# Kernel optimization log

Hardware: AMD Instinct MI355X
Metric: run time of the kernel (lower is better)

## Reference

```python
import jax, jax.numpy as jnp
import numpy as np

B, C, W, H, X, Y = 2, 32, 256, 256, 512, 512


def _rbf(x1, x2, ls):
    # x1: [B, N], x2: [B, M] -> [B, N, M]; identical math to norms+matmul pw_dists2 on 1-d coords
    d2 = (x1[:, :, None] - x2[:, None, :]) ** 2
    return jnp.exp(-0.5 * d2 / ls ** 2)


def setup_inputs() -> dict:
    key = jax.random.key(0)
    k0, k1, k2, k3, k4 = jax.random.split(key, 5)
    return {
        "x_in_lon": jax.random.uniform(k0, (B, W), jnp.float32),
        "x_in_lat": jax.random.uniform(k1, (B, H), jnp.float32),
        "wt": jax.random.normal(k2, (B, C, W, H), jnp.float32),
        "x_out_lon": jax.random.uniform(k3, (B, X), jnp.float32),
        "x_out_lat": jax.random.uniform(k4, (B, Y), jnp.float32),
        "init_ls": jnp.full((1,), 0.1, jnp.float32),
    }


def reference(x_in_lon, x_in_lat, wt, x_out_lon, x_out_lat, init_ls):
    # density channel: 1 where data present, 0 where NaN; zero-fill NaNs in data
    dens = jnp.where(jnp.isnan(wt[:, 0:1]), 0.0, 1.0)
    wt_full = jnp.concatenate([dens, jnp.nan_to_num(wt)], axis=1)  # [B, C+1, W, H]
    ls = init_ls[0]
    w_lon = _rbf(x_in_lon, x_out_lon, ls)  # [B, W, X]
    w_lat = _rbf(x_in_lat, x_out_lat, ls)  # [B, H, Y]
    # separable 'OnToOn' contraction: [B,C+1,W,H] x [B,W,X] x [B,H,Y] -> [B,C+1,X,Y]
    ee = jnp.einsum('bcwh,bwx,bhy->bcxy', wt_full, w_lon, w_lat)
    d = jnp.clip(ee[:, 0:1], 1e-6, 1e5)
    return jnp.concatenate([ee[:, 0:1], ee[:, 1:] / d], axis=1)
```

## Files before the change

### kernel.cpp

```cpp
#include <hip/hip_runtime.h>
#include <cstddef>

#define B_ 2
#define C_ 32
#define CP 33
#define W_ 256
#define H_ 256
#define X_ 512
#define Y_ 512

typedef __bf16 bf16x8 __attribute__((ext_vector_type(8)));
typedef __bf16 bf16x4 __attribute__((ext_vector_type(4)));
typedef float  f32x4  __attribute__((ext_vector_type(4)));

#define AS1 __attribute__((address_space(1)))
#define AS3 __attribute__((address_space(3)))

__device__ __forceinline__ void gload16_lds(const void* g, void* l) {
    __builtin_amdgcn_global_load_lds((const AS1 void*)g, (AS3 void*)l, 16, 0, 0);
}


__global__ __launch_bounds__(256) void prep_kernel(
    const float* __restrict__ xin_lon, const float* __restrict__ xin_lat,
    const float* __restrict__ xout_lon, const float* __restrict__ xout_lat,
    const float* __restrict__ init_ls, const float* __restrict__ wt,
    __bf16* __restrict__ wlonF, __bf16* __restrict__ wlatT,
    __bf16* __restrict__ wt33)
{
    const int NLONC = 32768;
    const int NLAT  = B_ * Y_ * H_;
    int t = blockIdx.x * 256 + threadIdx.x;
    float ls = init_ls[0];
    float cc = -0.5f / (ls * ls);
    if (t < NLONC) {
        int lane = t & 63, nf = (t >> 6) & 3, kt = (t >> 8) & 7;
        int xt = (t >> 11) & 7, b = t >> 14;
        int x  = xt * 64 + nf * 16 + (lane & 15);
        int k0 = kt * 32 + (lane >> 4) * 8;
        float xo = xout_lon[b * X_ + x];
        bf16x8 v;
#pragma unroll
        for (int e = 0; e < 8; ++e) {
            float d = xin_lon[b * W_ + k0 + e] - xo;
            v[e] = (__bf16)__expf(cc * d * d);
        }
        *(bf16x8*)&wlonF[(size_t)t * 8] = v;
    } else if (t < NLONC + NLAT) {
        int j = t - NLONC;
        int b = j / (Y_ * H_);
        int r = j - b * (Y_ * H_);
        int y = r >> 8;
        int h = r & (H_ - 1);
        float d = xin_lat[b * H_ + h] - xout_lat[b * Y_ + y];
        wlatT[j] = (__bf16)__expf(cc * d * d);
    } else {
        int j = t - (NLONC + NLAT);
        if (j >= (B_ * CP * W_ * H_) / 4) return;
        int o = j * 4;
        int b = o / (CP * W_ * H_);
        int r = o - b * (CP * W_ * H_);
        int co = r / (W_ * H_);
        int p = r & (W_ * H_ - 1);
        float4 v;
        bf16x4 ov;
        if (co == 0) {
            v = *(const float4*)&wt[((size_t)b * C_) * (W_ * H_) + p];
            ov[0] = (__bf16)((v.x != v.x) ? 0.f : 1.f);
            ov[1] = (__bf16)((v.y != v.y) ? 0.f : 1.f);
            ov[2] = (__bf16)((v.z != v.z) ? 0.f : 1.f);
            ov[3] = (__bf16)((v.w != v.w) ? 0.f : 1.f);
        } else {
            v = *(const float4*)&wt[((size_t)b * C_ + (co - 1)) * (W_ * H_) + p];
            ov[0] = (__bf16)((v.x != v.x) ? 0.f : v.x);
            ov[1] = (__bf16)((v.y != v.y) ? 0.f : v.y);
            ov[2] = (__bf16)((v.z != v.z) ? 0.f : v.z);
            ov[3] = (__bf16)((v.w != v.w) ? 0.f : v.w);
        }
        *(bf16x4*)&wt33[o] = ov;
    }
}

__global__ __launch_bounds__(256, 4) void gemm_u(
    const __bf16* __restrict__ wt33, const __bf16* __restrict__ wlatT,
    __bf16* __restrict__ U_F)
{
    __shared__ union SM {
        struct { __bf16 A[2][4096]; __bf16 Bt[2][2048]; } t;
        __bf16 th[8704];
    } sm;

    const int t    = threadIdx.x;
    const int lane = t & 63;
    const int wave = t >> 6;
    const int wm   = wave >> 1, wn = wave & 1;
    const int lrow = lane & 15, lkg = lane >> 4;

    const int xcd = blockIdx.x & 7, k = blockIdx.x >> 3;
    const int m   = xcd * 132 + k;
    const int p   = m >> 4, tile = m & 15;
    const int mtile = tile >> 3, ntile = tile & 7;
    const int bb = (p >= CP) ? 1 : 0;
    const __bf16* Abase = wt33 + (size_t)p * (W_ * H_) + (size_t)mtile * 128 * H_;
    const __bf16* Bbase = wlatT + (size_t)bb * (Y_ * H_) + (size_t)ntile * 64 * H_;

    auto stage = [&](int buf, int kt) {
#pragma unroll
        for (int j = 0; j < 2; ++j) {
            int f = j * 4 + wave;
            gload16_lds((const void*)(Abase + (f * 16 + lrow) * H_ + kt * 32 + lkg * 8),
                        (void*)&sm.t.A[buf][f * 512]);
        }
        gload16_lds((const void*)(Bbase + (wave * 16 + lrow) * H_ + kt * 32 + lkg * 8),
                    (void*)&sm.t.Bt[buf][wave * 512]);
    };

    f32x4 acc[4][2] = {};
    stage(0, 0);
#pragma unroll
    for (int kt = 0; kt < 8; ++kt) {
        const int buf = kt & 1;
        if (kt < 7) {
            stage(buf ^ 1, kt + 1);
            asm volatile("s_waitcnt vmcnt(3)" ::: "memory");
        } else {
            asm volatile("s_waitcnt vmcnt(0)" ::: "memory");
        }
        __builtin_amdgcn_s_barrier();
        bf16x8 af[4], bf[2];
#pragma unroll
        for (int mt = 0; mt < 4; ++mt)
            af[mt] = *(const bf16x8*)&sm.t.A[buf][((wm * 4 + mt) * 64 + lane) * 8];
#pragma unroll
        for (int nt = 0; nt < 2; ++nt)
            bf[nt] = *(const bf16x8*)&sm.t.Bt[buf][((wn * 2 + nt) * 64 + lane) * 8];
#pragma unroll
        for (int mt = 0; mt < 4; ++mt)
#pragma unroll
            for (int nt = 0; nt < 2; ++nt)
                acc[mt][nt] = __builtin_amdgcn_mfma_f32_16x16x32_bf16(
                    af[mt], bf[nt], acc[mt][nt], 0, 0, 0);
        __builtin_amdgcn_sched_barrier(0);
        __builtin_amdgcn_s_barrier();
    }

#pragma unroll
    for (int mt = 0; mt < 4; ++mt)
#pragma unroll
        for (int nt = 0; nt < 2; ++nt) {
            int yloc = wn * 32 + nt * 16 + lrow;
            int wloc = wm * 64 + mt * 16 + lkg * 4;
            f32x4 c = acc[mt][nt];
            bf16x4 v4;
            v4[0] = (__bf16)c[0]; v4[1] = (__bf16)c[1];
            v4[2] = (__bf16)c[2]; v4[3] = (__bf16)c[3];
            *(bf16x4*)&sm.th[yloc * 136 + wloc] = v4;
        }
    __syncthreads();
    __bf16* up = U_F + (size_t)p * 131072 + (size_t)ntile * 16384
                 + (size_t)mtile * 4 * 2048;
#pragma unroll
    for (int it = 0; it < 4; ++it) {
        int c2 = it * 256 + t;
        int ktl = c2 >> 8, rq = (c2 >> 6) & 3, ln = c2 & 63;
        int yloc = rq * 16 + (ln & 15);
        int w8   = ktl * 4 + (ln >> 4);
        bf16x8 v = *(const bf16x8*)&sm.th[yloc * 136 + w8 * 8];
        *(bf16x8*)&up[(size_t)(ktl * 4 + rq) * 512 + ln * 8] = v;
    }
}

__global__ __launch_bounds__(256, 2) void stage2_fused(
    const __bf16* __restrict__ wlonF, const __bf16* __restrict__ U_F,
    float* __restrict__ out)
{
    __shared__ __bf16 Ast[2][12288];

    const int t = threadIdx.x, lane = t & 63, wave = t >> 6;
    const int lrow = lane & 15, lkg = lane >> 4;
    const int wm = wave >> 1, wn = wave & 1;

    const int bid  = blockIdx.x;
    const int xcd  = bid & 7, q = bid >> 3;
    const int combo = (q >> 6) * 8 + xcd;
    const int b    = combo >> 3, g = combo & 7;
    const int tile = q & 63;
    const int yt   = tile >> 3, xt = tile & 7;
    const int x0   = xt * 64, y0 = yt * 64;

    const __bf16* lonF  = wlonF + (size_t)(b * 8 + xt) * 16384;
    const __bf16* Ubase = U_F + (size_t)(b * CP) * 131072 + (size_t)yt * 16384;

    auto stage = [&](int slot, int kt) {
#pragma unroll
        for (int i = 0; i < 6; ++i) {
            const int jf = wave * 6 + i;
            const __bf16* src;
            if (jf < 20) {
                const int jj = jf >> 2;
                const int ch = (jj == 0) ? 0 : (g * 4 + jj);
                src = Ubase + (size_t)ch * 131072
                      + (size_t)(kt * 4 + (jf & 3)) * 512 + lane * 8;
            } else {
                src = lonF + (size_t)(kt * 4 + (jf - 20)) * 512 + lane * 8;
            }
            gload16_lds((const void*)src, (void*)&Ast[slot][jf * 512]);
        }
    };

    stage(0, 0);

    f32x4 acc[5][2][2] = {};
#pragma unroll
    for (int kt = 0; kt < 8; ++kt) {
        const int slot = kt & 1;
        if (kt < 7) {
            stage(slot ^ 1, kt + 1);
            asm volatile("s_waitcnt vmcnt(6)" ::: "memory");
        } else {
            asm volatile("s_waitcnt vmcnt(0)" ::: "memory");
        }
        __builtin_amdgcn_s_barrier();
        bf16x8 af[5][2], bfv[2];
#pragma unroll
        for (int j = 0; j < 5; ++j)
#pragma unroll
            for (int mt = 0; mt < 2; ++mt)
                af[j][mt] = *(const bf16x8*)
                    &Ast[slot][((j * 4 + wm * 2 + mt) * 64 + lane) * 8];
#pragma unroll
        for (int nt = 0; nt < 2; ++nt)
            bfv[nt] = *(const bf16x8*)
                &Ast[slot][((20 + wn * 2 + nt) * 64 + lane) * 8];
        asm volatile("s_waitcnt lgkmcnt(0)" ::: "memory");
        __builtin_amdgcn_sched_barrier(0);
#pragma unroll
        for (int j = 0; j < 5; ++j)
#pragma unroll
            for (int mt = 0; mt < 2; ++mt)
#pragma unroll
                for (int nt = 0; nt < 2; ++nt)
                    acc[j][mt][nt] = __builtin_amdgcn_mfma_f32_16x16x32_bf16(
                        af[j][mt], bfv[nt], acc[j][mt][nt], 0, 0, 0);
        __builtin_amdgcn_sched_barrier(0);
        __builtin_amdgcn_s_barrier();
    }

    f32x4 rec[2][2];
#pragma unroll
    for (int mt = 0; mt < 2; ++mt)
#pragma unroll
        for (int nt = 0; nt < 2; ++nt) {
            f32x4 c = acc[0][mt][nt], q2;
#pragma unroll
            for (int rr = 0; rr < 4; ++rr)
                q2[rr] = 1.0f / fminf(fmaxf(c[rr], 1e-6f), 1e5f);
            rec[mt][nt] = q2;
        }
    if (g == 0) {
        float* outc = out + (size_t)(b * CP) * (X_ * Y_);
#pragma unroll
        for (int mt = 0; mt < 2; ++mt)
#pragma unroll
            for (int nt = 0; nt < 2; ++nt) {
                int xg = x0 + (wn * 2 + nt) * 16 + lrow;
                int yg = y0 + (wm * 2 + mt) * 16 + lkg * 4;
                *(f32x4*)&outc[(size_t)xg * Y_ + yg] = acc[0][mt][nt];
            }
    }
#pragma unroll
    for (int j = 1; j < 5; ++j) {
        float* outc = out + (size_t)(b * CP + g * 4 + j) * (size_t)(X_ * Y_);
#pragma unroll
        for (int mt = 0; mt < 2; ++mt)
#pragma unroll
            for (int nt = 0; nt < 2; ++nt) {
                int xg = x0 + (wn * 2 + nt) * 16 + lrow;
                int yg = y0 + (wm * 2 + mt) * 16 + lkg * 4;
                f32x4 v = acc[j][mt][nt] * rec[mt][nt];
                *(f32x4*)&outc[(size_t)xg * Y_ + yg] = v;
            }
    }
}

extern "C" void kernel_launch(void* const* d_in, const int* in_sizes, int n_in,
                              void* d_out, int out_size, void* d_ws, size_t ws_size,
                              hipStream_t stream)
{
    const float* xin_lon  = (const float*)d_in[0];
    const float* xin_lat  = (const float*)d_in[1];
    const float* wt       = (const float*)d_in[2];
    const float* xout_lon = (const float*)d_in[3];
    const float* xout_lat = (const float*)d_in[4];
    const float* init_ls  = (const float*)d_in[5];
    float* out = (float*)d_out;

    __bf16* wlonF = (__bf16*)d_ws;
    __bf16* wlatT = wlonF + (size_t)B_ * X_ * W_;
    __bf16* wt33  = wlatT + (size_t)B_ * Y_ * H_;
    __bf16* U_F   = wt33 + (size_t)B_ * CP * W_ * H_;

    prep_kernel<<<5376, 256, 0, stream>>>(xin_lon, xin_lat, xout_lon, xout_lat,
                                          init_ls, wt, wlonF, wlatT, wt33);
    gemm_u<<<1056, 256, 0, stream>>>(wt33, wlatT, U_F);
    stage2_fused<<<1024, 256, 0, stream>>>(wlonF, U_F, out);
}
```

Baseline: 53.25 us.

## Pre-swizzle wt and lat weights into MFMA fragment order for contiguous GEMM loads

The prep kernel now writes the bf16 input tensor and the latitude RBF weights directly in the fragment-tiled order the first GEMM consumes, using 8-element vector stores per thread. The GEMM's global-to-LDS loads then read fully contiguous 1 KB chunks per wave instead of strided row segments. The prep grid shrinks because each thread handles 8 elements. The cost is strided fp32 reads from wt in prep and more complex index math.

```diff
diff --git a/kernel.cpp b/kernel.cpp
--- a/kernel.cpp
+++ b/kernel.cpp
@@ -25,11 +25,11 @@
     const float* __restrict__ xin_lon, const float* __restrict__ xin_lat,
     const float* __restrict__ xout_lon, const float* __restrict__ xout_lat,
     const float* __restrict__ init_ls, const float* __restrict__ wt,
-    __bf16* __restrict__ wlonF, __bf16* __restrict__ wlatT,
-    __bf16* __restrict__ wt33)
+    __bf16* __restrict__ wlonF, __bf16* __restrict__ wlatF,
+    __bf16* __restrict__ wt33F)
 {
     const int NLONC = 32768;
-    const int NLAT  = B_ * Y_ * H_;
+    const int NLATC = 32768;
     int t = blockIdx.x * 256 + threadIdx.x;
     float ls = init_ls[0];
     float cc = -0.5f / (ls * ls);
@@ -46,43 +46,54 @@
             v[e] = (__bf16)__expf(cc * d * d);
         }
         *(bf16x8*)&wlonF[(size_t)t * 8] = v;
-    } else if (t < NLONC + NLAT) {
-        int j = t - NLONC;
-        int b = j / (Y_ * H_);
-        int r = j - b * (Y_ * H_);
-        int y = r >> 8;
-        int h = r & (H_ - 1);
-        float d = xin_lat[b * H_ + h] - xout_lat[b * Y_ + y];
-        wlatT[j] = (__bf16)__expf(cc * d * d);
+    } else if (t < NLONC + NLATC) {
+        int c = t - NLONC;
+        int lane = c & 63, bfr = (c >> 6) & 3, kt = (c >> 8) & 7;
+        int yt = (c >> 11) & 7, b = c >> 14;
+        int y  = yt * 64 + bfr * 16 + (lane & 15);
+        int h0 = kt * 32 + (lane >> 4) * 8;
+        float yo = xout_lat[b * Y_ + y];
+        bf16x8 v;
+#pragma unroll
+        for (int e = 0; e < 8; ++e) {
+            float d = xin_lat[b * H_ + h0 + e] - yo;
+            v[e] = (__bf16)__expf(cc * d * d);
+        }
+        *(bf16x8*)&wlatF[(size_t)c * 8] = v;
     } else {
-        int j = t - (NLONC + NLAT);
-        if (j >= (B_ * CP * W_ * H_) / 4) return;
-        int o = j * 4;
-        int b = o / (CP * W_ * H_);
-        int r = o - b * (CP * W_ * H_);
-        int co = r / (W_ * H_);
-        int p = r & (W_ * H_ - 1);
-        float4 v;
-        bf16x4 ov;
-        if (co == 0) {
-            v = *(const float4*)&wt[((size_t)b * C_) * (W_ * H_) + p];
-            ov[0] = (__bf16)((v.x != v.x) ? 0.f : 1.f);
-            ov[1] = (__bf16)((v.y != v.y) ? 0.f : 1.f);
-            ov[2] = (__bf16)((v.z != v.z) ? 0.f : 1.f);
-            ov[3] = (__bf16)((v.w != v.w) ? 0.f : 1.f);
+        int j = t - (NLONC + NLATC);
+        if (j >= 540672) return;
+        int p  = j >> 13;
+        int c2 = j & 8191;
+        int wtile = c2 >> 12, kt = (c2 >> 9) & 7, rf = (c2 >> 6) & 7, lane = c2 & 63;
+        int w  = wtile * 128 + rf * 16 + (lane & 15);
+        int h0 = kt * 32 + (lane >> 4) * 8;
+        int b  = p / CP, ch = p - b * CP;
+        bf16x8 ov;
+        if (ch == 0) {
+            const float* src = &wt[((size_t)b * C_) * (W_ * H_) + (size_t)w * H_ + h0];
+            float4 a0 = *(const float4*)src;
+            float4 a1 = *(const float4*)(src + 4);
+            float vv[8] = {a0.x, a0.y, a0.z, a0.w, a1.x, a1.y, a1.z, a1.w};
+#pragma unroll
+            for (int e = 0; e < 8; ++e)
+                ov[e] = (__bf16)((vv[e] != vv[e]) ? 0.f : 1.f);
         } else {
-            v = *(const float4*)&wt[((size_t)b * C_ + (co - 1)) * (W_ * H_) + p];
-            ov[0] = (__bf16)((v.x != v.x) ? 0.f : v.x);
-            ov[1] = (__bf16)((v.y != v.y) ? 0.f : v.y);
-            ov[2] = (__bf16)((v.z != v.z) ? 0.f : v.z);
-            ov[3] = (__bf16)((v.w != v.w) ? 0.f : v.w);
-        }
-        *(bf16x4*)&wt33[o] = ov;
+            const float* src = &wt[((size_t)b * C_ + (ch - 1)) * (W_ * H_)
+                                   + (size_t)w * H_ + h0];
+            float4 a0 = *(const float4*)src;
+            float4 a1 = *(const float4*)(src + 4);
+            float vv[8] = {a0.x, a0.y, a0.z, a0.w, a1.x, a1.y, a1.z, a1.w};
+#pragma unroll
+            for (int e = 0; e < 8; ++e)
+                ov[e] = (__bf16)((vv[e] != vv[e]) ? 0.f : vv[e]);
+        }
+        *(bf16x8*)&wt33F[(size_t)j * 8] = ov;
     }
 }
 
 __global__ __launch_bounds__(256, 4) void gemm_u(
-    const __bf16* __restrict__ wt33, const __bf16* __restrict__ wlatT,
+    const __bf16* __restrict__ wt33F, const __bf16* __restrict__ wlatF,
     __bf16* __restrict__ U_F)
 {
     __shared__ union SM {
@@ -101,17 +112,17 @@
     const int p   = m >> 4, tile = m & 15;
     const int mtile = tile >> 3, ntile = tile & 7;
     const int bb = (p >= CP) ? 1 : 0;
-    const __bf16* Abase = wt33 + (size_t)p * (W_ * H_) + (size_t)mtile * 128 * H_;
-    const __bf16* Bbase = wlatT + (size_t)bb * (Y_ * H_) + (size_t)ntile * 64 * H_;
+    const __bf16* Abase = wt33F + ((size_t)(p * 2 + mtile)) * 32768;
+    const __bf16* Bbase = wlatF + ((size_t)(bb * 8 + ntile)) * 16384;
 
     auto stage = [&](int buf, int kt) {
 #pragma unroll
         for (int j = 0; j < 2; ++j) {
-            int f = j * 4 + wave;
-            gload16_lds((const void*)(Abase + (f * 16 + lrow) * H_ + kt * 32 + lkg * 8),
-                        (void*)&sm.t.A[buf][f * 512]);
-        }
-        gload16_lds((const void*)(Bbase + (wave * 16 + lrow) * H_ + kt * 32 + lkg * 8),
+            int rf = j * 4 + wave;
+            gload16_lds((const void*)(Abase + (size_t)(kt * 8 + rf) * 512 + lane * 8),
+                        (void*)&sm.t.A[buf][rf * 512]);
+        }
+        gload16_lds((const void*)(Bbase + (size_t)(kt * 4 + wave) * 512 + lane * 8),
                     (void*)&sm.t.Bt[buf][wave * 512]);
     };
 
@@ -296,12 +307,12 @@
     float* out = (float*)d_out;
 
     __bf16* wlonF = (__bf16*)d_ws;
-    __bf16* wlatT = wlonF + (size_t)B_ * X_ * W_;
-    __bf16* wt33  = wlatT + (size_t)B_ * Y_ * H_;
-    __bf16* U_F   = wt33 + (size_t)B_ * CP * W_ * H_;
-
-    prep_kernel<<<5376, 256, 0, stream>>>(xin_lon, xin_lat, xout_lon, xout_lat,
-                                          init_ls, wt, wlonF, wlatT, wt33);
-    gemm_u<<<1056, 256, 0, stream>>>(wt33, wlatT, U_F);
+    __bf16* wlatF = wlonF + (size_t)B_ * X_ * W_;
+    __bf16* wt33F = wlatF + (size_t)B_ * Y_ * H_;
+    __bf16* U_F   = wt33F + (size_t)B_ * CP * W_ * H_;
+
+    prep_kernel<<<2368, 256, 0, stream>>>(xin_lon, xin_lat, xout_lon, xout_lat,
+                                          init_ls, wt, wlonF, wlatF, wt33F);
+    gemm_u<<<1056, 256, 0, stream>>>(wt33F, wlatF, U_F);
     stage2_fused<<<1024, 256, 0, stream>>>(wlonF, U_F, out);
 }
```

Result: faster. 46.18 us (-13.3%).
